# Optimization experiments

Hardware: AMD Instinct MI355X
Metric: run time of the kernel (lower is better)

The kernel has to match this reference:

```python
import jax, jax.numpy as jnp
import numpy as np
from jax import lax

# dims
B, T, C, V, L = 4, 1024, 1024, 32000, 2
NR, NT, E = 6, 2, 8          # rwkv experts, transformer experts, total
HID = 4 * C                  # FFN hidden
P, R = 8, 64                 # bridge prefix_len, low_rank_dim
NH, HD = 16, 64              # heads, head_size


def _layernorm(x, g, b, eps=1e-5):
    m = jnp.mean(x, axis=-1, keepdims=True)
    v = jnp.var(x, axis=-1, keepdims=True)
    return (x - m) * lax.rsqrt(v + eps) * g + b


def setup_inputs() -> dict:
    key = jax.random.key(0)
    ks = list(jax.random.split(key, 32))
    it = iter(ks)
    def nrm(shape, s=0.02):
        return jax.random.normal(next(it), shape, dtype=jnp.float32) * s
    inp = {}
    inp['idx'] = jax.random.randint(next(it), (B, T), 0, V)
    inp['capital_shares'] = jax.random.uniform(next(it), (L, E), dtype=jnp.float32)
    inp['emb'] = nrm((V, C), 1.0)
    inp['head'] = nrm((C, V))
    inp['ln1_g'] = jnp.ones((L, C), jnp.float32)
    inp['ln1_b'] = jnp.zeros((L, C), jnp.float32)
    inp['ln2_g'] = jnp.ones((L, C), jnp.float32)
    inp['ln2_b'] = jnp.zeros((L, C), jnp.float32)
    inp['lno_g'] = jnp.ones((C,), jnp.float32)
    inp['lno_b'] = jnp.zeros((C,), jnp.float32)
    inp['att_Wr'] = nrm((L, C, C))
    inp['att_Wk'] = nrm((L, C, C))
    inp['att_Wv'] = nrm((L, C, C))
    inp['att_Wo'] = nrm((L, C, C))
    inp['att_decay'] = nrm((L, C), 1.0)
    inp['critic_wd'] = nrm((L, C))
    inp['critic_Wa'] = nrm((L, C, E))
    inp['bridge_Wdown'] = nrm((C, R))
    inp['bridge_Wup'] = nrm((P, R, C))
    inp['eWk'] = nrm((L, NR, C, HID))
    inp['eWv'] = nrm((L, NR, HID, C))
    inp['conf_r'] = nrm((L, NR, C))
    inp['tWq'] = nrm((L, NT, C, C))
    inp['tWk'] = nrm((L, NT, C, C))
    inp['tWv'] = nrm((L, NT, C, C))
    inp['tWo'] = nrm((L, NT, C, C))
    inp['conf_t'] = nrm((L, NT, C))
    return inp


def _forward(idx, capital_shares, emb, head, ln1_g, ln1_b, ln2_g, ln2_b,
             lno_g, lno_b, att_Wr, att_Wk, att_Wv, att_Wo, att_decay,
             critic_wd, critic_Wa, bridge_Wdown, bridge_Wup,
             eWk, eWv, conf_r, tWq, tWk, tWv, tWo, conf_t):
    x = emb[idx]                                   # [B,T,C]
    v_first = jnp.zeros_like(x)
    for l in range(L):
        # --- TimeMix (simplified RWKV: per-channel decayed kv state) ---
        x_ln = _layernorm(x, ln1_g[l], ln1_b[l])
        r = jax.nn.sigmoid(x_ln @ att_Wr[l])       # [B,T,C]
        k = x_ln @ att_Wk[l]
        v = x_ln @ att_Wv[l]
        if l == 0:
            v_first = v
        else:
            v = 0.5 * (v + v_first)
        w = jax.nn.sigmoid(att_decay[l])           # [C] decay in (0,1)
        def step(s, kv):
            kt, vt = kv
            s = w * s + kt * vt
            return s, s
        kT = jnp.swapaxes(k, 0, 1)                 # [T,B,C]
        vT = jnp.swapaxes(v, 0, 1)
        _, s_seq = lax.scan(step, jnp.zeros((B, C), x.dtype), (kT, vT))
        rwkv_state = jnp.swapaxes(s_seq, 0, 1)     # [B,T,C]
        att_out = (r * rwkv_state) @ att_Wo[l]
        x = x + att_out
        # --- routing (market) ---
        h = _layernorm(x, ln2_g[l], ln2_b[l])
        conf_rw = jax.nn.sigmoid(jnp.einsum('btc,ec->bte', h, conf_r[l]))
        conf_tr = jax.nn.sigmoid(jnp.einsum('btc,ec->bte', h, conf_t[l]))
        confidences = jnp.concatenate([conf_rw, conf_tr], axis=-1)  # [B,T,E]
        difficulty = jax.nn.softplus(jnp.einsum('btc,c->bt', h, critic_wd[l]))[..., None]
        affinity = jnp.einsum('btc,ce->bte', h, critic_Wa[l])
        subsidy = jnp.tanh(affinity)               # critic.apply_to_bids(0, affinity)
        bids = confidences * capital_shares[l] * difficulty + subsidy
        top2_vals, winners = lax.top_k(bids, 2)    # [B,T,2]
        weights = jax.nn.softmax(top2_vals, axis=-1)
        gate = (weights[..., 0:1] * jax.nn.one_hot(winners[..., 0], E, dtype=h.dtype)
                + weights[..., 1:2] * jax.nn.one_hot(winners[..., 1], E, dtype=h.dtype))  # [B,T,E]
        # --- bridge prefix (low-rank, shared) ---
        flat_h = h.reshape(-1, C)
        flat_state = rwkv_state.reshape(-1, C)
        u = (flat_h + flat_state) @ bridge_Wdown   # [N,R]
        prefix = jnp.einsum('nr,prc->npc', u, bridge_Wup)  # [N,P,C]
        # --- experts: dense-equivalent of gather/compute/scatter ---
        final = jnp.zeros_like(h)
        for e in range(NR):                        # squared-relu FFN experts
            hid = jnp.square(jax.nn.relu(h @ eWk[l, e]))
            final = final + gate[..., e:e + 1] * (hid @ eWv[l, e])
        scale = 1.0 / jnp.sqrt(jnp.float32(HD))
        for j in range(NT):                        # linear transformer experts over prefix
            q = (flat_h @ tWq[l, j]).reshape(-1, NH, HD)
            kp = (prefix @ tWk[l, j]).reshape(-1, P, NH, HD)
            vp = (prefix @ tWv[l, j]).reshape(-1, P, NH, HD)
            attn = jax.nn.softmax(jnp.einsum('nhd,nphd->nhp', q, kp) * scale, axis=-1)
            o = jnp.einsum('nhp,nphd->nhd', attn, vp).reshape(-1, C) @ tWo[l, j]
            final = final + gate[..., NR + j:NR + j + 1] * o.reshape(B, T, C)
        x = x + final
    x = _layernorm(x, lno_g, lno_b)
    return x @ head                                # [B,T,V] logits


def reference(idx, capital_shares, emb, head, ln1_g, ln1_b, ln2_g, ln2_b,
              lno_g, lno_b, att_Wr, att_Wk, att_Wv, att_Wo, att_decay,
              critic_wd, critic_Wa, bridge_Wdown, bridge_Wup,
              eWk, eWv, conf_r, tWq, tWk, tWv, tWo, conf_t):
    return _forward(idx, capital_shares, emb, head, ln1_g, ln1_b, ln2_g, ln2_b,
                    lno_g, lno_b, att_Wr, att_Wk, att_Wv, att_Wo, att_decay,
                    critic_wd, critic_Wa, bridge_Wdown, bridge_Wup,
                    eWk, eWv, conf_r, tWq, tWk, tWv, tWo, conf_t)
```

## Files before the change

kernel.cpp:

```cpp
#include <hip/hip_runtime.h>

typedef _Float16 h16;
typedef __attribute__((ext_vector_type(8))) _Float16 h16x8;
typedef __attribute__((ext_vector_type(4))) _Float16 h16x4;
typedef __attribute__((ext_vector_type(4))) float f32x4;

#define DEVFN static __device__ __forceinline__

DEVFN void gl_lds16(const void* g, void* l) {
  __builtin_amdgcn_global_load_lds((const __attribute__((address_space(1))) unsigned int*)g,
                                   (__attribute__((address_space(3))) unsigned int*)l, 16, 0, 0);
}
DEVFN void fsplit(float v, h16& hi, h16& lo) { hi = (h16)v; lo = (h16)(v - (float)hi); }
DEVFN float wred(float v) {
  #pragma unroll
  for (int m = 32; m >= 1; m >>= 1) v += __shfl_xor(v, m, 64);
  return v;
}
DEVFN float sigm(float x) { return 1.0f / (1.0f + expf(-x)); }
DEVFN float softpl(float x) { return fmaxf(x, 0.0f) + log1pf(expf(-fabsf(x))); }

enum { EPI_WRITE = 0, EPI_ADD = 1, EPI_SQRELU = 3, EPI_TSPLIT = 4, EPI_SCATTER = 5 };

template<bool SPLIT, int EPI, int MODE>
__global__ __launch_bounds__(256, 2) void gemm_k(
    const h16* __restrict__ Ah, const h16* __restrict__ Al, long lda, long sAz,
    const h16* __restrict__ Bh, const h16* __restrict__ Bl, long ldb, long sBz,
    float* __restrict__ C, long ldc, long sCz,
    h16* __restrict__ Oh, h16* __restrict__ Ol, long ldo,
    int K, int nmask, const float* __restrict__ rs, int rsStride,
    const int4* __restrict__ meta, int metaStep,
    const int* __restrict__ lists, int listStep, long sOz)
{
  __shared__ h16 As[(SPLIT ? 2 : 1) * 4096];
  __shared__ h16 Bs[(SPLIT ? 2 : 1) * 4096];
  const int tid = threadIdx.x;
  const int lane = tid & 63, wave = tid >> 6;
  const int wr = wave >> 1, wc = wave & 1;
  const long z = blockIdx.z;
  const long m0 = (long)blockIdx.x * 128, n0 = (long)blockIdx.y * 128;

  int cntv = 0;
  long koff = 0;
  const int* lst = nullptr;
  if (MODE == 1) {
    const int4 mt = meta[z * metaStep];
    if ((int)m0 >= mt.y) return;
    cntv = mt.x; lst = lists + z * listStep;
  } else if (MODE == 2) {
    const int4 mt = meta[0];
    if ((int)m0 >= mt.y) return;
    cntv = mt.x; lst = lists; koff = z * (long)K;
  }

  const h16* pAh = Ah + z * sAz;
  const h16* pBh = Bh + z * sBz;
  const h16* pAl = SPLIT ? (Al + z * sAz) : nullptr;
  const h16* pBl = SPLIT ? (Bl + z * sBz) : nullptr;
  const int rA = wave * 16 + (lane >> 2);
  const int khalf = (lane & 3) * 8;
  long arow0, arow1;
  if (MODE == 1) { arow0 = lst[m0 + rA]; arow1 = lst[m0 + rA + 64]; }
  else           { arow0 = m0 + rA; arow1 = arow0 + 64; }
  const long aoff0 = arow0 * lda + khalf + koff;
  const long aoff1 = arow1 * lda + khalf + koff;
  const long boff = (n0 + rA) * ldb + khalf + koff;
  h16* lA = &As[wave * 512];
  h16* lB = &Bs[wave * 512];
  const int fr = lane & 15, fq = lane >> 4;

  const f32x4 zero = {0.f, 0.f, 0.f, 0.f};
  f32x4 acc[4][4];
  #pragma unroll
  for (int m = 0; m < 4; m++)
    #pragma unroll
    for (int n = 0; n < 4; n++) acc[m][n] = zero;

  for (int k0 = 0; k0 < K; k0 += 32) {
    gl_lds16(pAh + aoff0 + k0, lA);
    gl_lds16(pAh + aoff1 + k0, lA + 2048);
    gl_lds16(pBh + boff + k0, lB);
    gl_lds16(pBh + boff + k0 + 64 * ldb, lB + 2048);
    if (SPLIT) {
      gl_lds16(pAl + aoff0 + k0, lA + 4096);
      gl_lds16(pAl + aoff1 + k0, lA + 4096 + 2048);
      gl_lds16(pBl + boff + k0, lB + 4096);
      gl_lds16(pBl + boff + k0 + 64 * ldb, lB + 4096 + 2048);
    }
    __syncthreads();
    h16x8 af[4], bf[4], afl[4], bfl[4];
    #pragma unroll
    for (int m = 0; m < 4; m++) {
      const int r = (wr * 64 + m * 16 + fr) * 32 + fq * 8;
      af[m] = *(const h16x8*)&As[r];
      if (SPLIT) afl[m] = *(const h16x8*)&As[4096 + r];
    }
    #pragma unroll
    for (int n = 0; n < 4; n++) {
      const int r = (wc * 64 + n * 16 + fr) * 32 + fq * 8;
      bf[n] = *(const h16x8*)&Bs[r];
      if (SPLIT) bfl[n] = *(const h16x8*)&Bs[4096 + r];
    }
    #pragma unroll
    for (int m = 0; m < 4; m++)
      #pragma unroll
      for (int n = 0; n < 4; n++) {
        acc[m][n] = __builtin_amdgcn_mfma_f32_16x16x32_f16(af[m], bf[n], acc[m][n], 0, 0, 0);
        if (SPLIT) {
          acc[m][n] = __builtin_amdgcn_mfma_f32_16x16x32_f16(af[m], bfl[n], acc[m][n], 0, 0, 0);
          acc[m][n] = __builtin_amdgcn_mfma_f32_16x16x32_f16(afl[m], bf[n], acc[m][n], 0, 0, 0);
        }
      }
    __syncthreads();
  }

  #pragma unroll
  for (int m = 0; m < 4; m++) {
    const long lrow = m0 + wr * 64 + m * 16 + fq * 4;
    #pragma unroll
    for (int n = 0; n < 4; n++) {
      const long gcol = n0 + wc * 64 + n * 16 + fr;
      if (nmask && gcol >= nmask) continue;
      if (EPI == EPI_TSPLIT) {
        h16x4 hv, lv;
        #pragma unroll
        for (int i = 0; i < 4; i++) { h16 a, b2; fsplit(acc[m][n][i], a, b2); hv[i] = a; lv[i] = b2; }
        *(h16x4*)&Oh[z * sOz + gcol * ldo + lrow] = hv;
        *(h16x4*)&Ol[z * sOz + gcol * ldo + lrow] = lv;
      } else if (EPI == EPI_SCATTER) {
        #pragma unroll
        for (int i = 0; i < 4; i++) {
          const int slot = (int)lrow + i;
          if (slot >= cntv) continue;
          const int tok = lst[slot];
          const float g = rs[(long)tok * rsStride];
          atomicAdd(&C[(long)tok * ldc + gcol], g * acc[m][n][i]);
        }
      } else {
        float* cp = C + z * sCz + lrow * ldc + gcol;
        #pragma unroll
        for (int i = 0; i < 4; i++) {
          const float v = acc[m][n][i];
          if (EPI == EPI_WRITE) cp[i * ldc] = v;
          else cp[i * ldc] += v;
        }
      }
    }
  }
}

template<bool SPLIT, int EPI, int MODE>
__global__ __launch_bounds__(512, 1) void gemm256_k(
    const h16* __restrict__ Ah, const h16* __restrict__ Al, long lda,
    const h16* __restrict__ Bh, const h16* __restrict__ Bl, long ldb, long sBz,
    float* __restrict__ C, long ldc,
    h16* __restrict__ Oh, h16* __restrict__ Ol, long ldo,
    int K, const float* __restrict__ rs, int rsStride,
    const int4* __restrict__ meta, const int* __restrict__ lists, int listStep,
    const int* __restrict__ mmap)
{
  __shared__ h16 As[(SPLIT ? 2 : 1) * 8192];
  __shared__ h16 Bs[(SPLIT ? 2 : 1) * 8192];
  const int tid = threadIdx.x;
  const int lane = tid & 63, wave = tid >> 6;
  const int wr = wave >> 2, wc = wave & 3;
  const long m0 = (long)blockIdx.x * 256, n0 = (long)blockIdx.y * 256;

  int cntv = 0, eIdx = 0, eOff = 0;
  long koff = 0;
  const int* lst = nullptr;
  if (MODE == 3 || MODE == 4) {
    if ((int)m0 >= meta[8].x) return;
    eIdx = mmap[blockIdx.x];
    const int4 mt = meta[eIdx];
    cntv = mt.x; eOff = mt.z;
    lst = lists + eIdx * listStep;
    if (MODE == 4) koff = blockIdx.z * (long)K;
  }

  const h16* pAh = Ah;
  const h16* pBh = Bh + (long)eIdx * sBz;
  const h16* pAl = SPLIT ? Al : nullptr;
  const h16* pBl = SPLIT ? (Bl + (long)eIdx * sBz) : nullptr;
  const int rA = (tid >> 2) & 127;
  const int khalf = (lane & 3) * 8;
  long arow0, arow1;
  if (MODE == 3) { arow0 = lst[m0 + rA - eOff]; arow1 = lst[m0 + rA + 128 - eOff]; }
  else           { arow0 = m0 + rA; arow1 = arow0 + 128; }
  const long aoff0 = arow0 * lda + khalf + koff;
  const long aoff1 = arow1 * lda + khalf + koff;
  const long boff0 = (n0 + rA) * ldb + khalf + koff;
  const long boff1 = boff0 + 128 * ldb;
  h16* lA = &As[wave * 512];
  h16* lB = &Bs[wave * 512];
  const int fr = lane & 15, fq = lane >> 4;

  const f32x4 zero = {0.f, 0.f, 0.f, 0.f};
  f32x4 acc[8][4];
  #pragma unroll
  for (int m = 0; m < 8; m++)
    #pragma unroll
    for (int n = 0; n < 4; n++) acc[m][n] = zero;

  for (int k0 = 0; k0 < K; k0 += 32) {
    gl_lds16(pAh + aoff0 + k0, lA);
    gl_lds16(pAh + aoff1 + k0, lA + 4096);
    gl_lds16(pBh + boff0 + k0, lB);
    gl_lds16(pBh + boff1 + k0, lB + 4096);
    if (SPLIT) {
      gl_lds16(pAl + aoff0 + k0, lA + 8192);
      gl_lds16(pAl + aoff1 + k0, lA + 8192 + 4096);
      gl_lds16(pBl + boff0 + k0, lB + 8192);
      gl_lds16(pBl + boff1 + k0, lB + 8192 + 4096);
    }
    __syncthreads();
    h16x8 bf[4], bfl[4];
    #pragma unroll
    for (int n = 0; n < 4; n++) {
      const int r = (wc * 64 + n * 16 + fr) * 32 + fq * 8;
      bf[n] = *(const h16x8*)&Bs[r];
      if (SPLIT) bfl[n] = *(const h16x8*)&Bs[8192 + r];
    }
    #pragma unroll
    for (int m = 0; m < 8; m++) {
      const int r = (wr * 128 + m * 16 + fr) * 32 + fq * 8;
      const h16x8 af = *(const h16x8*)&As[r];
      h16x8 afl;
      if (SPLIT) afl = *(const h16x8*)&As[8192 + r];
      #pragma unroll
      for (int n = 0; n < 4; n++) {
        acc[m][n] = __builtin_amdgcn_mfma_f32_16x16x32_f16(af, bf[n], acc[m][n], 0, 0, 0);
        if (SPLIT) {
          acc[m][n] = __builtin_amdgcn_mfma_f32_16x16x32_f16(af, bfl[n], acc[m][n], 0, 0, 0);
          acc[m][n] = __builtin_amdgcn_mfma_f32_16x16x32_f16(afl, bf[n], acc[m][n], 0, 0, 0);
        }
      }
    }
    __syncthreads();
  }

  #pragma unroll
  for (int m = 0; m < 8; m++) {
    const long lrow = m0 + wr * 128 + m * 16 + fq * 4;
    #pragma unroll
    for (int n = 0; n < 4; n++) {
      const long gcol = n0 + wc * 64 + n * 16 + fr;
      if (EPI == EPI_SQRELU) {
        #pragma unroll
        for (int i = 0; i < 4; i++) {
          float v = acc[m][n][i];
          v = v > 0.f ? v * v : 0.f;
          const h16 a = (h16)v;
          Oh[(lrow + i) * ldo + gcol] = a;
          if (Ol) Ol[(lrow + i) * ldo + gcol] = (h16)(v - (float)a);
        }
      } else if (EPI == EPI_SCATTER) {
        #pragma unroll
        for (int i = 0; i < 4; i++) {
          const int slot = (int)lrow + i - eOff;
          if (slot >= cntv) continue;
          const int tok = lst[slot];
          atomicAdd(&C[(long)tok * ldc + gcol], rs[(long)tok * rsStride + eIdx] * acc[m][n][i]);
        }
      } else {
        float* cp = C + lrow * ldc + gcol;
        #pragma unroll
        for (int i = 0; i < 4; i++) cp[i * ldc] = acc[m][n][i];
      }
    }
  }
}

template<bool LO>
__global__ __launch_bounds__(256) void k_tsplit(
    const float* __restrict__ in, long inZ,
    h16* __restrict__ oh, h16* __restrict__ ol, long outZ, int Kd, int Nd)
{
  __shared__ float t[64][65];
  const long z = blockIdx.z;
  in += z * inZ; oh += z * outZ; if (LO) ol += z * outZ;
  const int n0 = blockIdx.x * 64, k0 = blockIdx.y * 64;
  const int tr = threadIdx.x >> 4, tc = threadIdx.x & 15;
  #pragma unroll
  for (int r = 0; r < 4; r++) {
    const int row = r * 16 + tr;
    const float4 v = *(const float4*)&in[(long)(k0 + row) * Nd + n0 + tc * 4];
    t[row][tc * 4 + 0] = v.x; t[row][tc * 4 + 1] = v.y;
    t[row][tc * 4 + 2] = v.z; t[row][tc * 4 + 3] = v.w;
  }
  __syncthreads();
  #pragma unroll
  for (int r = 0; r < 4; r++) {
    const int nrow = r * 16 + tr;
    h16x4 hv, lv;
    #pragma unroll
    for (int i = 0; i < 4; i++) {
      h16 a, b2; fsplit(t[tc * 4 + i][nrow], a, b2);
      hv[i] = a; lv[i] = b2;
    }
    *(h16x4*)&oh[(long)(n0 + nrow) * Kd + k0 + tc * 4] = hv;
    if (LO) *(h16x4*)&ol[(long)(n0 + nrow) * Kd + k0 + tc * 4] = lv;
  }
}

template<bool LO>
__global__ __launch_bounds__(256) void k_tsplit4(
    const float* __restrict__ s0, const float* __restrict__ s1,
    const float* __restrict__ s2, const float* __restrict__ s3,
    long inAdd, h16* __restrict__ oh, h16* __restrict__ ol, int Kd, int Nd)
{
  __shared__ float t[64][65];
  const int z = blockIdx.z;
  const long seg = (long)Kd * Nd;
  const int w = z & 3;
  const float* in = (w == 0 ? s0 : w == 1 ? s1 : w == 2 ? s2 : s3) + (inAdd + (z >> 2)) * seg;
  oh += (long)z * seg; if (LO) ol += (long)z * seg;
  const int n0 = blockIdx.x * 64, k0 = blockIdx.y * 64;
  const int tr = threadIdx.x >> 4, tc = threadIdx.x & 15;
  #pragma unroll
  for (int r = 0; r < 4; r++) {
    const int row = r * 16 + tr;
    const float4 v = *(const float4*)&in[(long)(k0 + row) * Nd + n0 + tc * 4];
    t[row][tc * 4 + 0] = v.x; t[row][tc * 4 + 1] = v.y;
    t[row][tc * 4 + 2] = v.z; t[row][tc * 4 + 3] = v.w;
  }
  __syncthreads();
  #pragma unroll
  for (int r = 0; r < 4; r++) {
    const int nrow = r * 16 + tr;
    h16x4 hv, lv;
    #pragma unroll
    for (int i = 0; i < 4; i++) {
      h16 a, b2; fsplit(t[tc * 4 + i][nrow], a, b2);
      hv[i] = a; lv[i] = b2;
    }
    *(h16x4*)&oh[(long)(n0 + nrow) * Kd + k0 + tc * 4] = hv;
    if (LO) *(h16x4*)&ol[(long)(n0 + nrow) * Kd + k0 + tc * 4] = lv;
  }
}

__global__ void k_split(const float* __restrict__ in, h16* __restrict__ oh, h16* __restrict__ ol)
{
  const long i = (long)blockIdx.x * 256 + threadIdx.x;
  const float4 v = ((const float4*)in)[i];
  h16x4 hv, lv; h16 a, b2;
  fsplit(v.x, a, b2); hv[0] = a; lv[0] = b2;
  fsplit(v.y, a, b2); hv[1] = a; lv[1] = b2;
  fsplit(v.z, a, b2); hv[2] = a; lv[2] = b2;
  fsplit(v.w, a, b2); hv[3] = a; lv[3] = b2;
  ((h16x4*)oh)[i] = hv; ((h16x4*)ol)[i] = lv;
}

__global__ void k_embed(const int* __restrict__ idx, const float* __restrict__ emb, float* __restrict__ x)
{
  const int row = blockIdx.x;
  const long e = (long)idx[row] * 1024;
  ((float4*)(x + (long)row * 1024))[threadIdx.x] = ((const float4*)(emb + e))[threadIdx.x];
}

__global__ __launch_bounds__(256) void k_ln(
    const float* __restrict__ x, const float* __restrict__ g, const float* __restrict__ b,
    float* __restrict__ yf, h16* __restrict__ yh, h16* __restrict__ yl)
{
  const int row = blockIdx.x, tid = threadIdx.x;
  const float4 v = ((const float4*)(x + (long)row * 1024))[tid];
  __shared__ float red[4];
  const int wv = tid >> 6;
  float s = wred(v.x + v.y + v.z + v.w);
  if ((tid & 63) == 0) red[wv] = s;
  __syncthreads();
  const float mean = (red[0] + red[1] + red[2] + red[3]) * (1.0f / 1024.0f);
  const float d0 = v.x - mean, d1 = v.y - mean, d2 = v.z - mean, d3 = v.w - mean;
  float s2 = wred(d0 * d0 + d1 * d1 + d2 * d2 + d3 * d3);
  __syncthreads();
  if ((tid & 63) == 0) red[wv] = s2;
  __syncthreads();
  const float var = (red[0] + red[1] + red[2] + red[3]) * (1.0f / 1024.0f);
  const float rstd = 1.0f / sqrtf(var + 1e-5f);
  const float4 gv = ((const float4*)g)[tid];
  const float4 bv = ((const float4*)b)[tid];
  const float y0 = d0 * rstd * gv.x + bv.x;
  const float y1 = d1 * rstd * gv.y + bv.y;
  const float y2 = d2 * rstd * gv.z + bv.z;
  const float y3 = d3 * rstd * gv.w + bv.w;
  if (yf) { float4 o; o.x = y0; o.y = y1; o.z = y2; o.w = y3; ((float4*)(yf + (long)row * 1024))[tid] = o; }
  h16x4 hv, lv; h16 a, b2;
  fsplit(y0, a, b2); hv[0] = a; lv[0] = b2;
  fsplit(y1, a, b2); hv[1] = a; lv[1] = b2;
  fsplit(y2, a, b2); hv[2] = a; lv[2] = b2;
  fsplit(y3, a, b2); hv[3] = a; lv[3] = b2;
  *(h16x4*)(yh + (long)row * 1024 + tid * 4) = hv;
  if (yl) *(h16x4*)(yl + (long)row * 1024 + tid * 4) = lv;
}

__global__ void k_vfix(float* __restrict__ rkv, float* __restrict__ vfir, int mode)
{
  const int row = blockIdx.x, tid = threadIdx.x;
  float4* vp = (float4*)(rkv + (long)row * 3072 + 2048) + tid;
  float4* fp = (float4*)(vfir + (long)row * 1024) + tid;
  if (mode == 0) *fp = *vp;
  else {
    float4 a = *vp; const float4 b = *fp;
    a.x = 0.5f * (a.x + b.x); a.y = 0.5f * (a.y + b.y);
    a.z = 0.5f * (a.z + b.z); a.w = 0.5f * (a.w + b.w);
    *vp = a;
  }
}

__global__ __launch_bounds__(256) void k_scan1(const float* __restrict__ rkv,
                                               const float* __restrict__ dec, float* __restrict__ carry)
{
  const int gid = blockIdx.x * 256 + threadIdx.x;
  const int c = gid & 1023, bb = (gid >> 10) & 3, ch = gid >> 12;
  const float w = sigm(dec[c]);
  float s = 0.f;
  const long base = ((long)bb * 1024 + ch * 64) * 3072 + c;
  const float* kp_ = rkv + 1024 + base;
  const float* vp_ = rkv + 2048 + base;
  for (int t = 0; t < 64; t++) s = w * s + kp_[(long)t * 3072] * vp_[(long)t * 3072];
  carry[(ch * 4 + bb) * 1024 + c] = s;
}
__global__ void k_scan2(const float* __restrict__ dec, float* __restrict__ carry)
{
  const int gid = blockIdx.x * 256 + threadIdx.x;
  const int c = gid & 1023, bb = gid >> 10;
  const float w = sigm(dec[c]);
  float w64 = w;
  for (int i = 0; i < 6; i++) w64 *= w64;
  float s = 0.f;
  for (int j = 0; j < 16; j++) {
    const int o = (j * 4 + bb) * 1024 + c;
    const float a = carry[o];
    carry[o] = s;
    s = w64 * s + a;
  }
}
__global__ __launch_bounds__(256) void k_scan3(const float* __restrict__ rkv,
                                               const float* __restrict__ dec, const float* __restrict__ carry,
                                               float* __restrict__ st)
{
  const int gid = blockIdx.x * 256 + threadIdx.x;
  const int c = gid & 1023, bb = (gid >> 10) & 3, ch = gid >> 12;
  const float w = sigm(dec[c]);
  float s = carry[(ch * 4 + bb) * 1024 + c];
  const long base = ((long)bb * 1024 + ch * 64) * 3072 + c;
  const float* kp_ = rkv + 1024 + base;
  const float* vp_ = rkv + 2048 + base;
  float* so = st + ((long)bb * 1024 + ch * 64) * 1024 + c;
  for (int t = 0; t < 64; t++) {
    s = w * s + kp_[(long)t * 3072] * vp_[(long)t * 3072];
    so[(long)t * 1024] = s;
  }
}

__global__ void k_attin(const float* __restrict__ rkv, const float* __restrict__ s,
                        h16* __restrict__ oh, h16* __restrict__ ol)
{
  const int row = blockIdx.x, tid = threadIdx.x;
  const float4 rv = *((const float4*)(rkv + (long)row * 3072) + tid);
  const float4 sv = *((const float4*)(s + (long)row * 1024) + tid);
  h16x4 hv, lv; h16 a, b2;
  fsplit(sv.x * sigm(rv.x), a, b2); hv[0] = a; lv[0] = b2;
  fsplit(sv.y * sigm(rv.y), a, b2); hv[1] = a; lv[1] = b2;
  fsplit(sv.z * sigm(rv.z), a, b2); hv[2] = a; lv[2] = b2;
  fsplit(sv.w * sigm(rv.w), a, b2); hv[3] = a; lv[3] = b2;
  const long i = (long)row * 256 + tid;
  ((h16x4*)oh)[i] = hv; ((h16x4*)ol)[i] = lv;
}

__global__ void k_addsplit(const float* __restrict__ p, const float* __restrict__ q,
                           h16* __restrict__ oh, h16* __restrict__ ol)
{
  const long i = (long)blockIdx.x * 256 + threadIdx.x;
  const float4 av = ((const float4*)p)[i];
  const float4 bv = ((const float4*)q)[i];
  h16x4 hv, lv; h16 a, b2;
  fsplit(av.x + bv.x, a, b2); hv[0] = a; lv[0] = b2;
  fsplit(av.y + bv.y, a, b2); hv[1] = a; lv[1] = b2;
  fsplit(av.z + bv.z, a, b2); hv[2] = a; lv[2] = b2;
  fsplit(av.w + bv.w, a, b2); hv[3] = a; lv[3] = b2;
  ((h16x4*)oh)[i] = hv; ((h16x4*)ol)[i] = lv;
}

__global__ __launch_bounds__(256) void k_route(
    const float* __restrict__ h, const float* __restrict__ cr, const float* __restrict__ ct,
    const float* __restrict__ wd, const float* __restrict__ wa,
    const float* __restrict__ cap, float* __restrict__ gate)
{
  const int wv = threadIdx.x >> 6, ln = threadIdx.x & 63;
  const int row = blockIdx.x * 4 + wv;
  const float* hr = h + (long)row * 1024;
  float hreg[16];
  #pragma unroll
  for (int i = 0; i < 4; i++) {
    const float4 t = ((const float4*)hr)[ln * 4 + i];
    hreg[i * 4 + 0] = t.x; hreg[i * 4 + 1] = t.y; hreg[i * 4 + 2] = t.z; hreg[i * 4 + 3] = t.w;
  }
  float dots[17];
  #pragma unroll
  for (int e = 0; e < 6; e++) {
    float p = 0.f;
    #pragma unroll
    for (int j = 0; j < 16; j++) p += hreg[j] * cr[e * 1024 + ln * 16 + j];
    dots[e] = p;
  }
  #pragma unroll
  for (int e = 0; e < 2; e++) {
    float p = 0.f;
    #pragma unroll
    for (int j = 0; j < 16; j++) p += hreg[j] * ct[e * 1024 + ln * 16 + j];
    dots[6 + e] = p;
  }
  {
    float p = 0.f;
    #pragma unroll
    for (int j = 0; j < 16; j++) p += hreg[j] * wd[ln * 16 + j];
    dots[8] = p;
  }
  #pragma unroll
  for (int e = 0; e < 8; e++) {
    float p = 0.f;
    #pragma unroll
    for (int j = 0; j < 16; j++) p += hreg[j] * wa[(ln * 16 + j) * 8 + e];
    dots[9 + e] = p;
  }
  #pragma unroll
  for (int d = 0; d < 17; d++) dots[d] = wred(dots[d]);
  if (ln == 0) {
    float bids[8];
    const float diff = softpl(dots[8]);
    #pragma unroll
    for (int e = 0; e < 6; e++) bids[e] = sigm(dots[e]) * cap[e] * diff + tanhf(dots[9 + e]);
    #pragma unroll
    for (int e = 0; e < 2; e++) bids[6 + e] = sigm(dots[6 + e]) * cap[6 + e] * diff + tanhf(dots[15 + e]);
    int w0 = 0;
    for (int e = 1; e < 8; e++) if (bids[e] > bids[w0]) w0 = e;
    int w1 = -1;
    for (int e = 0; e < 8; e++) if (e != w0 && (w1 < 0 || bids[e] > bids[w1])) w1 = e;
    const float e1 = expf(bids[w1] - bids[w0]);
    const float q0 = 1.0f / (1.0f + e1), q1 = e1 / (1.0f + e1);
    for (int e = 0; e < 8; e++) gate[(long)row * 8 + e] = (e == w0) ? q0 : ((e == w1) ? q1 : 0.0f);
  }
}

__global__ void k_build(const float* __restrict__ gate, int* __restrict__ cnt, int* __restrict__ lists)
{
  const int t = blockIdx.x * 256 + threadIdx.x;
  #pragma unroll
  for (int e = 0; e < 8; e++)
    if (gate[(long)t * 8 + e] > 0.f) { const int s = atomicAdd(&cnt[e], 1); lists[e * 4224 + s] = t; }
}
__global__ void k_meta(const int* __restrict__ cnt, int4* __restrict__ meta, int* __restrict__ lists,
                       int* __restrict__ mmap)
{
  __shared__ int sc[8], sp[8], so[8];
  if (threadIdx.x == 0) {
    int acc = 0;
    for (int e = 0; e < 8; e++) {
      const int c = cnt[e], p = (c + 255) & ~255;
      sc[e] = c; sp[e] = p; so[e] = (e < 6) ? acc : 0;
      if (e < 6) acc += p;
    }
    meta[8] = make_int4(acc, 0, 0, 0);
    for (int b = 0; b < 64; b++) mmap[b] = 0;
    for (int e = 0; e < 6; e++)
      for (int b = so[e] >> 8; b < (so[e] + sp[e]) >> 8; b++) mmap[b] = e;
  }
  __syncthreads();
  const int e = threadIdx.x >> 5, i = threadIdx.x & 31;
  for (int s = sc[e] + i; s < sp[e]; s += 32) lists[e * 4224 + s] = 0;
  if (i == 0) meta[e] = make_int4(sc[e], sp[e], so[e], 0);
}

__global__ __launch_bounds__(256) void k_scores(const float* __restrict__ q, const float* __restrict__ kp,
                                                float* __restrict__ attn, const int4* __restrict__ meta)
{
  const int gw = blockIdx.x * 4 + (threadIdx.x >> 6), ln = threadIdx.x & 63;
  const int n = gw >> 4, hh = gw & 15;
  if (n >= meta->y) return;
  const float qv = q[(long)n * 1024 + hh * 64 + ln];
  float s[8];
  #pragma unroll
  for (int p = 0; p < 8; p++) {
    float t = qv * kp[(long)n * 8192 + p * 1024 + hh * 64 + ln];
    s[p] = wred(t) * 0.125f;
  }
  if (ln == 0) {
    float mx = s[0];
    #pragma unroll
    for (int p = 1; p < 8; p++) mx = fmaxf(mx, s[p]);
    float ex[8], sum = 0.f;
    #pragma unroll
    for (int p = 0; p < 8; p++) { ex[p] = expf(s[p] - mx); sum += ex[p]; }
    const float inv = 1.0f / sum;
    #pragma unroll
    for (int p = 0; p < 8; p++) attn[(long)n * 128 + hh * 8 + p] = ex[p] * inv;
  }
}

__global__ void k_omix(const float* __restrict__ attn, const float* __restrict__ vp,
                       h16* __restrict__ oh, h16* __restrict__ ol, const int4* __restrict__ meta)
{
  const long gid = (long)blockIdx.x * 256 + threadIdx.x;
  const int n = gid >> 10, hd = gid & 1023, hh = hd >> 6;
  if (n >= meta->y) return;
  const float* a = attn + (long)n * 128 + hh * 8;
  float o = 0.f;
  #pragma unroll
  for (int p = 0; p < 8; p++) o += a[p] * vp[(long)n * 8192 + p * 1024 + hd];
  h16 hi, lo; fsplit(o, hi, lo);
  oh[gid] = hi; ol[gid] = lo;
}

#define GEMM3(SPL, EPI, MODE, GRID, ...) do { \
  if (SPL) gemm_k<true,  EPI, MODE><<<GRID, 256, 0, stream>>>(__VA_ARGS__); \
  else     gemm_k<false, EPI, MODE><<<GRID, 256, 0, stream>>>(__VA_ARGS__); } while (0)
#define GEMM256(SPL, EPI, MODE, GRID, ...) do { \
  if (SPL) gemm256_k<true,  EPI, MODE><<<GRID, 512, 0, stream>>>(__VA_ARGS__); \
  else     gemm256_k<false, EPI, MODE><<<GRID, 512, 0, stream>>>(__VA_ARGS__); } while (0)

extern "C" void kernel_launch(void* const* d_in, const int* in_sizes, int n_in,
                              void* d_out, int out_size, void* d_ws, size_t ws_size,
                              hipStream_t stream)
{
  (void)in_sizes; (void)n_in; (void)out_size; (void)ws_size;
  const int*   idx   = (const int*)  d_in[0];
  const float* cap   = (const float*)d_in[1];
  const float* emb   = (const float*)d_in[2];
  const float* headw = (const float*)d_in[3];
  const float* ln1g  = (const float*)d_in[4];
  const float* ln1b  = (const float*)d_in[5];
  const float* ln2g  = (const float*)d_in[6];
  const float* ln2b  = (const float*)d_in[7];
  const float* lnog  = (const float*)d_in[8];
  const float* lnob  = (const float*)d_in[9];
  const float* aWr   = (const float*)d_in[10];
  const float* aWk   = (const float*)d_in[11];
  const float* aWv   = (const float*)d_in[12];
  const float* aWo   = (const float*)d_in[13];
  const float* adec  = (const float*)d_in[14];
  const float* cwd   = (const float*)d_in[15];
  const float* cWa   = (const float*)d_in[16];
  const float* bWd   = (const float*)d_in[17];
  const float* bWu   = (const float*)d_in[18];
  const float* eWkw  = (const float*)d_in[19];
  const float* eWvw  = (const float*)d_in[20];
  const float* confr = (const float*)d_in[21];
  const float* tWq   = (const float*)d_in[22];
  const float* tWkk  = (const float*)d_in[23];
  const float* tWv   = (const float*)d_in[24];
  const float* tWo   = (const float*)d_in[25];
  const float* conft = (const float*)d_in[26];
  float* out = (float*)d_out;

  char* ws = (char*)d_ws;
  size_t off = 0;
  auto alloc = [&](size_t n) -> char* {
    off = (off + 255) & ~(size_t)255;
    char* p = ws + off; off += n; return p;
  };
  const long M1 = 1048576, M4 = 4194304;

  h16* attWh = (h16*)alloc(8 * M1 * 2);
  h16* attWl = (h16*)alloc(8 * M1 * 2);
  h16* eWkh  = (h16*)alloc(12 * M4 * 2);
  h16* eWkl  = (h16*)alloc(6 * M4 * 2);
  h16* eWvh  = (h16*)alloc(12 * M4 * 2);
  h16* eWvl  = (h16*)alloc(6 * M4 * 2);
  h16* tWh   = (h16*)alloc(16 * M1 * 2);
  h16* headh = (h16*)alloc(32768000ull * 2);
  h16* wdh   = (h16*)alloc(131072 * 2);
  h16* wuph  = (h16*)alloc(524288 * 2);
  h16* wupl  = (h16*)alloc(524288 * 2);
  h16* wukth = (h16*)alloc(524288 * 2);
  h16* wuvth = (h16*)alloc(524288 * 2);
  h16* wuktl = (h16*)alloc(524288 * 2);
  h16* wuvtl = (h16*)alloc(524288 * 2);
  h16* s1h   = (h16*)alloc(M4 * 2);
  h16* s1l   = (h16*)alloc(M4 * 2);
  h16* hh_   = (h16*)alloc(M4 * 2);
  h16* hl_   = (h16*)alloc(M4 * 2);
  h16* uh    = (h16*)alloc(262144 * 2);
  h16* ul    = (h16*)alloc(262144 * 2);
  float* x    = (float*)alloc(M4 * 4);
  float* vfir = (float*)alloc(M4 * 4);
  float* rkv  = (float*)alloc(3 * M4 * 4);
  float* st   = (float*)alloc(M4 * 4);
  float* hf   = (float*)alloc(M4 * 4);
  float* qf   = (float*)alloc(M4 * 4);
  char* big   = alloc(167772160);
  h16* hidh   = (h16*)big;
  h16* hidl   = (h16*)(big + 83886080ull);
  float* kp   = (float*)big;
  float* carry = (float*)alloc(65536 * 4);
  float* gate  = (float*)alloc(32768 * 4);
  float* uf    = (float*)alloc(262144 * 4);
  float* attn  = (float*)alloc(524288 * 4);
  int*   cnt8  = (int*)alloc(32);
  int4*  metaA = (int4*)alloc(16 * 16);
  int*   lists = (int*)alloc(8 * 4224 * 4);
  int*   mmap  = (int*)alloc(64 * 4);

  k_tsplit4<true><<<dim3(16, 16, 8), 256, 0, stream>>>(aWr, aWk, aWv, aWo, 0, attWh, attWl, 1024, 1024);
  k_tsplit<true ><<<dim3(64, 16, 6), 256, 0, stream>>>(eWkw, M4, eWkh, eWkl, M4, 1024, 4096);
  k_tsplit<false><<<dim3(64, 16, 6), 256, 0, stream>>>(eWkw + 6 * M4, M4, eWkh + 6 * M4, nullptr, M4, 1024, 4096);
  k_tsplit<true ><<<dim3(16, 64, 6), 256, 0, stream>>>(eWvw, M4, eWvh, eWvl, M4, 4096, 1024);
  k_tsplit<false><<<dim3(16, 64, 6), 256, 0, stream>>>(eWvw + 6 * M4, M4, eWvh + 6 * M4, nullptr, M4, 4096, 1024);
  k_tsplit4<false><<<dim3(16, 16, 16), 256, 0, stream>>>(tWq, tWkk, tWv, tWo, 0, tWh, nullptr, 1024, 1024);
  k_tsplit<false><<<dim3(500, 16, 1), 256, 0, stream>>>(headw, 0, headh, nullptr, 0, 1024, 32000);
  k_tsplit<false><<<dim3(1, 16, 1), 256, 0, stream>>>(bWd, 0, wdh, nullptr, 0, 1024, 64);
  hipMemsetAsync(wdh + 65536, 0, 65536 * 2, stream);
  k_split<<<512, 256, 0, stream>>>(bWu, wuph, wupl);

  k_embed<<<4096, 256, 0, stream>>>(idx, emb, x);

  for (int l = 0; l < 2; l++) {
    const bool SE = (l == 0);
    k_ln<<<4096, 256, 0, stream>>>(x, ln1g + l * 1024, ln1b + l * 1024, nullptr, s1h, s1l);
    GEMM3(true, EPI_WRITE, 0, dim3(32, 24),
          s1h, s1l, 1024, 0, attWh + (l * 4) * M1, attWl + (l * 4) * M1, 1024, 0,
          rkv, 3072, 0, nullptr, nullptr, 0, 1024, 0, nullptr, 0, nullptr, 0, nullptr, 0, 0);
    k_vfix<<<4096, 256, 0, stream>>>(rkv, vfir, l == 0 ? 0 : 1);
    k_scan1<<<256, 256, 0, stream>>>(rkv, adec + l * 1024, carry);
    k_scan2<<<16, 256, 0, stream>>>(adec + l * 1024, carry);
    k_scan3<<<256, 256, 0, stream>>>(rkv, adec + l * 1024, carry, st);
    k_attin<<<4096, 256, 0, stream>>>(rkv, st, s1h, s1l);
    GEMM3(true, EPI_ADD, 0, dim3(32, 8),
          s1h, s1l, 1024, 0, attWh + (l * 4 + 3) * M1, attWl + (l * 4 + 3) * M1, 1024, 0,
          x, 1024, 0, nullptr, nullptr, 0, 1024, 0, nullptr, 0, nullptr, 0, nullptr, 0, 0);
    k_ln<<<4096, 256, 0, stream>>>(x, ln2g + l * 1024, ln2b + l * 1024, hf, hh_, hl_);
    k_route<<<1024, 256, 0, stream>>>(hf, confr + l * 6144, conft + l * 2048, cwd + l * 1024, cWa + l * 8192, cap + l * 8, gate);
    hipMemsetAsync(cnt8, 0, 32, stream);
    k_build<<<16, 256, 0, stream>>>(gate, cnt8, lists);
    k_meta<<<1, 256, 0, stream>>>(cnt8, metaA, lists, mmap);
    k_addsplit<<<4096, 256, 0, stream>>>(hf, st, s1h, s1l);
    GEMM3(false, EPI_WRITE, 0, dim3(32, 1),
          s1h, nullptr, 1024, 0, wdh, nullptr, 1024, 0,
          uf, 64, 0, nullptr, nullptr, 0, 1024, 64, nullptr, 0, nullptr, 0, nullptr, 0, 0);
    k_split<<<256, 256, 0, stream>>>(uf, uh, ul);
    GEMM256(SE, EPI_SQRELU, 3, dim3(40, 16),
            hh_, hl_, 1024, eWkh + l * 6 * M4, eWkl, 1024, M4,
            nullptr, 0, hidh, SE ? hidl : nullptr, 4096,
            1024, nullptr, 0, metaA, lists, 4224, mmap);
    GEMM256(SE, EPI_SCATTER, 4, dim3(40, 4, 4),
            hidh, hidl, 4096, eWvh + l * 6 * M4, eWvl, 4096, M4,
            x, 1024, nullptr, nullptr, 0,
            1024, gate, 8, metaA, lists, 4224, mmap);
    for (int j = 0; j < 2; j++) {
      const long wi = (l * 2 + j) * 4;
      const int4* mt = metaA + 6 + j;
      const int* lstT = lists + (6 + j) * 4224;
      GEMM3(false, EPI_TSPLIT, 0, dim3(4, 8, 2),
            wuph, nullptr, 1024, 0, tWh + (wi + 1) * M1, nullptr, 1024, M1,
            nullptr, 0, 0, wukth, wuktl, 512, 1024, 0, nullptr, 0, nullptr, 0, nullptr, 0, 524288);
      GEMM3(false, EPI_WRITE, 1, dim3(32, 8),
            hh_, nullptr, 1024, 0, tWh + (wi + 0) * M1, nullptr, 1024, 0,
            qf, 1024, 0, nullptr, nullptr, 0, 1024, 0, nullptr, 0, mt, 0, lstT, 0, 0);
      GEMM3(false, EPI_WRITE, 1, dim3(32, 8, 8),
            uh, nullptr, 64, 0, wukth, nullptr, 512, 64,
            kp, 8192, 1024, nullptr, nullptr, 0, 64, 0, nullptr, 0, mt, 0, lstT, 0, 0);
      k_scores<<<16384, 256, 0, stream>>>(qf, kp, attn, mt);
      GEMM3(false, EPI_WRITE, 1, dim3(32, 8, 8),
            uh, nullptr, 64, 0, wuvth, nullptr, 512, 64,
            kp, 8192, 1024, nullptr, nullptr, 0, 64, 0, nullptr, 0, mt, 0, lstT, 0, 0);
      k_omix<<<16384, 256, 0, stream>>>(attn, kp, s1h, s1l, mt);
      GEMM3(false, EPI_SCATTER, 2, dim3(32, 8, 4),
            s1h, nullptr, 1024, 0, tWh + (wi + 3) * M1, nullptr, 1024, 0,
            x, 1024, 0, nullptr, nullptr, 0, 256, 0, gate + 6 + j, 8, mt, 0, lstT, 0, 0);
    }
  }

  k_ln<<<4096, 256, 0, stream>>>(x, lnog, lnob, nullptr, s1h, s1l);
  GEMM3(false, EPI_WRITE, 0, dim3(32, 250),
        s1h, nullptr, 1024, 0, headh, nullptr, 1024, 0,
        out, 32000, 0, nullptr, nullptr, 0, 1024, 0, nullptr, 0, nullptr, 0, nullptr, 0, 0);
}
```

Measured before the change: 2.954 ms.

## Batch both transformer experts into single launches with fp16 intermediates

Replaces the per-expert loop for the two transformer experts with batched GEMM launches that cover both experts through new grid-z modes, which cut the number of kernel launches and raise the number of blocks per launch. The prefix K/V projections are now written as fp16 instead of fp32, and the attention output is stored as fp16 only, with no hi/lo split. The RWKV down-projection split-K count is also doubled. The fp16 storage of K, V and the attention output lowers precision, and the change adds more atomic scatter traffic.

New measurement: 3.184 ms. 1.08x slower.

```diff
diff --git a/kernel.cpp b/kernel.cpp
--- a/kernel.cpp
+++ b/kernel.cpp
@@ -20,7 +20,7 @@
 DEVFN float sigm(float x) { return 1.0f / (1.0f + expf(-x)); }
 DEVFN float softpl(float x) { return fmaxf(x, 0.0f) + log1pf(expf(-fabsf(x))); }
 
-enum { EPI_WRITE = 0, EPI_ADD = 1, EPI_SQRELU = 3, EPI_TSPLIT = 4, EPI_SCATTER = 5 };
+enum { EPI_WRITE = 0, EPI_ADD = 1, EPI_SQRELU = 3, EPI_TSPLIT = 4, EPI_SCATTER = 5, EPI_WRITEH = 6 };
 
 template<bool SPLIT, int EPI, int MODE>
 __global__ __launch_bounds__(256, 2) void gemm_k(
@@ -40,7 +40,7 @@
   const long z = blockIdx.z;
   const long m0 = (long)blockIdx.x * 128, n0 = (long)blockIdx.y * 128;
 
-  int cntv = 0;
+  int cntv = 0, eSel = 0;
   long koff = 0;
   const int* lst = nullptr;
   if (MODE == 1) {
@@ -51,20 +51,36 @@
     const int4 mt = meta[0];
     if ((int)m0 >= mt.y) return;
     cntv = mt.x; lst = lists; koff = z * (long)K;
-  }
-
-  const h16* pAh = Ah + z * sAz;
-  const h16* pBh = Bh + z * sBz;
-  const h16* pAl = SPLIT ? (Al + z * sAz) : nullptr;
-  const h16* pBl = SPLIT ? (Bl + z * sBz) : nullptr;
+  } else if (MODE == 5) {
+    eSel = (int)(z >> 2);
+    const int4 mt = meta[eSel * metaStep];
+    if ((int)m0 >= mt.y) return;
+    cntv = mt.x; lst = lists + eSel * listStep;
+    koff = (long)(z & 3) * K;
+  } else if (MODE == 6) {
+    eSel = (int)(z >> 3);
+    const int4 mt = meta[eSel * metaStep];
+    if ((int)m0 >= mt.y) return;
+    cntv = mt.x; lst = lists + eSel * listStep;
+  }
+
+  long zA = z, zB = z;
+  if (MODE == 5) { zA = eSel; zB = eSel; }
+  else if (MODE == 6) { zA = eSel; }
+  const h16* pAh = Ah + zA * sAz;
+  const h16* pBh = Bh + zB * sBz;
+  const h16* pAl = SPLIT ? (Al + zA * sAz) : nullptr;
+  const h16* pBl = SPLIT ? (Bl + zB * sBz) : nullptr;
   const int rA = wave * 16 + (lane >> 2);
   const int khalf = (lane & 3) * 8;
   long arow0, arow1;
-  if (MODE == 1) { arow0 = lst[m0 + rA]; arow1 = lst[m0 + rA + 64]; }
-  else           { arow0 = m0 + rA; arow1 = arow0 + 64; }
-  const long aoff0 = arow0 * lda + khalf + koff;
-  const long aoff1 = arow1 * lda + khalf + koff;
+  if (MODE == 1 || MODE == 6) { arow0 = lst[m0 + rA]; arow1 = lst[m0 + rA + 64]; }
+  else if (MODE == 5)         { arow0 = m0 + rA; arow1 = arow0 + 64; }
+  else                        { arow0 = m0 + rA; arow1 = arow0 + 64; }
+  const long aoff0 = arow0 * lda + khalf + (MODE == 5 ? 0 : koff);
+  const long aoff1 = arow1 * lda + khalf + (MODE == 5 ? 0 : koff);
   const long boff = (n0 + rA) * ldb + khalf + koff;
+  const long aoffk = (MODE == 5 ? koff : 0);
   h16* lA = &As[wave * 512];
   h16* lB = &Bs[wave * 512];
   const int fr = lane & 15, fq = lane >> 4;
@@ -77,13 +93,13 @@
     for (int n = 0; n < 4; n++) acc[m][n] = zero;
 
   for (int k0 = 0; k0 < K; k0 += 32) {
-    gl_lds16(pAh + aoff0 + k0, lA);
-    gl_lds16(pAh + aoff1 + k0, lA + 2048);
+    gl_lds16(pAh + aoff0 + aoffk + k0, lA);
+    gl_lds16(pAh + aoff1 + aoffk + k0, lA + 2048);
     gl_lds16(pBh + boff + k0, lB);
     gl_lds16(pBh + boff + k0 + 64 * ldb, lB + 2048);
     if (SPLIT) {
-      gl_lds16(pAl + aoff0 + k0, lA + 4096);
-      gl_lds16(pAl + aoff1 + k0, lA + 4096 + 2048);
+      gl_lds16(pAl + aoff0 + aoffk + k0, lA + 4096);
+      gl_lds16(pAl + aoff1 + aoffk + k0, lA + 4096 + 2048);
       gl_lds16(pBl + boff + k0, lB + 4096);
       gl_lds16(pBl + boff + k0 + 64 * ldb, lB + 4096 + 2048);
     }
@@ -127,13 +143,17 @@
         for (int i = 0; i < 4; i++) { h16 a, b2; fsplit(acc[m][n][i], a, b2); hv[i] = a; lv[i] = b2; }
         *(h16x4*)&Oh[z * sOz + gcol * ldo + lrow] = hv;
         *(h16x4*)&Ol[z * sOz + gcol * ldo + lrow] = lv;
+      } else if (EPI == EPI_WRITEH) {
+        #pragma unroll
+        for (int i = 0; i < 4; i++)
+          Oh[z * sOz + (lrow + i) * ldo + gcol] = (h16)acc[m][n][i];
       } else if (EPI == EPI_SCATTER) {
         #pragma unroll
         for (int i = 0; i < 4; i++) {
           const int slot = (int)lrow + i;
           if (slot >= cntv) continue;
           const int tok = lst[slot];
-          const float g = rs[(long)tok * rsStride];
+          const float g = rs[(long)tok * rsStride + (MODE == 5 ? eSel : 0)];
           atomicAdd(&C[(long)tok * ldc + gcol], g * acc[m][n][i]);
         }
       } else {
@@ -572,7 +592,7 @@
   if (i == 0) meta[e] = make_int4(sc[e], sp[e], so[e], 0);
 }
 
-__global__ __launch_bounds__(256) void k_scores(const float* __restrict__ q, const float* __restrict__ kp,
+__global__ __launch_bounds__(256) void k_scores(const float* __restrict__ q, const h16* __restrict__ kp,
                                                 float* __restrict__ attn, const int4* __restrict__ meta)
 {
   const int gw = blockIdx.x * 4 + (threadIdx.x >> 6), ln = threadIdx.x & 63;
@@ -582,7 +602,7 @@
   float s[8];
   #pragma unroll
   for (int p = 0; p < 8; p++) {
-    float t = qv * kp[(long)n * 8192 + p * 1024 + hh * 64 + ln];
+    float t = qv * (float)kp[(long)p * 4194304 + (long)n * 1024 + hh * 64 + ln];
     s[p] = wred(t) * 0.125f;
   }
   if (ln == 0) {
@@ -598,8 +618,8 @@
   }
 }
 
-__global__ void k_omix(const float* __restrict__ attn, const float* __restrict__ vp,
-                       h16* __restrict__ oh, h16* __restrict__ ol, const int4* __restrict__ meta)
+__global__ void k_omix2(const float* __restrict__ attn, const h16* __restrict__ vp,
+                        h16* __restrict__ oh, const int4* __restrict__ meta)
 {
   const long gid = (long)blockIdx.x * 256 + threadIdx.x;
   const int n = gid >> 10, hd = gid & 1023, hh = hd >> 6;
@@ -607,9 +627,8 @@
   const float* a = attn + (long)n * 128 + hh * 8;
   float o = 0.f;
   #pragma unroll
-  for (int p = 0; p < 8; p++) o += a[p] * vp[(long)n * 8192 + p * 1024 + hd];
-  h16 hi, lo; fsplit(o, hi, lo);
-  oh[gid] = hi; ol[gid] = lo;
+  for (int p = 0; p < 8; p++) o += a[p] * (float)vp[(long)p * 4194304 + (long)n * 1024 + hd];
+  oh[gid] = (h16)o;
 }
 
 #define GEMM3(SPL, EPI, MODE, GRID, ...) do { \
@@ -672,11 +691,11 @@
   h16* wdh   = (h16*)alloc(131072 * 2);
   h16* wuph  = (h16*)alloc(524288 * 2);
   h16* wupl  = (h16*)alloc(524288 * 2);
-  h16* wukth = (h16*)alloc(524288 * 2);
-  h16* wuvth = (h16*)alloc(524288 * 2);
-  h16* wuktl = (h16*)alloc(524288 * 2);
-  h16* wuvtl = (h16*)alloc(524288 * 2);
-  h16* s1h   = (h16*)alloc(M4 * 2);
+  h16* foldKh = (h16*)alloc(1048576 * 2);
+  h16* foldKl = (h16*)alloc(1048576 * 2);
+  h16* foldVh = (h16*)alloc(1048576 * 2);
+  h16* foldVl = (h16*)alloc(1048576 * 2);
+  h16* s1h   = (h16*)alloc(2 * M4 * 2);
   h16* s1l   = (h16*)alloc(M4 * 2);
   h16* hh_   = (h16*)alloc(M4 * 2);
   h16* hl_   = (h16*)alloc(M4 * 2);
@@ -687,15 +706,15 @@
   float* rkv  = (float*)alloc(3 * M4 * 4);
   float* st   = (float*)alloc(M4 * 4);
   float* hf   = (float*)alloc(M4 * 4);
-  float* qf   = (float*)alloc(M4 * 4);
+  float* qf   = (float*)alloc(2 * M4 * 4);
   char* big   = alloc(167772160);
   h16* hidh   = (h16*)big;
   h16* hidl   = (h16*)(big + 83886080ull);
-  float* kp   = (float*)big;
+  h16* kpH    = (h16*)big;
   float* carry = (float*)alloc(65536 * 4);
   float* gate  = (float*)alloc(32768 * 4);
   float* uf    = (float*)alloc(262144 * 4);
-  float* attn  = (float*)alloc(524288 * 4);
+  float* attn  = (float*)alloc(2 * 524288 * 4);
   int*   cnt8  = (int*)alloc(32);
   int4*  metaA = (int4*)alloc(16 * 16);
   int*   lists = (int*)alloc(8 * 4224 * 4);
@@ -742,32 +761,38 @@
             hh_, hl_, 1024, eWkh + l * 6 * M4, eWkl, 1024, M4,
             nullptr, 0, hidh, SE ? hidl : nullptr, 4096,
             1024, nullptr, 0, metaA, lists, 4224, mmap);
-    GEMM256(SE, EPI_SCATTER, 4, dim3(40, 4, 4),
+    GEMM256(SE, EPI_SCATTER, 4, dim3(40, 4, 8),
             hidh, hidl, 4096, eWvh + l * 6 * M4, eWvl, 4096, M4,
             x, 1024, nullptr, nullptr, 0,
-            1024, gate, 8, metaA, lists, 4224, mmap);
-    for (int j = 0; j < 2; j++) {
-      const long wi = (l * 2 + j) * 4;
-      const int4* mt = metaA + 6 + j;
-      const int* lstT = lists + (6 + j) * 4224;
-      GEMM3(false, EPI_TSPLIT, 0, dim3(4, 8, 2),
-            wuph, nullptr, 1024, 0, tWh + (wi + 1) * M1, nullptr, 1024, M1,
-            nullptr, 0, 0, wukth, wuktl, 512, 1024, 0, nullptr, 0, nullptr, 0, nullptr, 0, 524288);
-      GEMM3(false, EPI_WRITE, 1, dim3(32, 8),
-            hh_, nullptr, 1024, 0, tWh + (wi + 0) * M1, nullptr, 1024, 0,
-            qf, 1024, 0, nullptr, nullptr, 0, 1024, 0, nullptr, 0, mt, 0, lstT, 0, 0);
-      GEMM3(false, EPI_WRITE, 1, dim3(32, 8, 8),
-            uh, nullptr, 64, 0, wukth, nullptr, 512, 64,
-            kp, 8192, 1024, nullptr, nullptr, 0, 64, 0, nullptr, 0, mt, 0, lstT, 0, 0);
-      k_scores<<<16384, 256, 0, stream>>>(qf, kp, attn, mt);
-      GEMM3(false, EPI_WRITE, 1, dim3(32, 8, 8),
-            uh, nullptr, 64, 0, wuvth, nullptr, 512, 64,
-            kp, 8192, 1024, nullptr, nullptr, 0, 64, 0, nullptr, 0, mt, 0, lstT, 0, 0);
-      k_omix<<<16384, 256, 0, stream>>>(attn, kp, s1h, s1l, mt);
-      GEMM3(false, EPI_SCATTER, 2, dim3(32, 8, 4),
-            s1h, nullptr, 1024, 0, tWh + (wi + 3) * M1, nullptr, 1024, 0,
-            x, 1024, 0, nullptr, nullptr, 0, 256, 0, gate + 6 + j, 8, mt, 0, lstT, 0, 0);
-    }
+            512, gate, 8, metaA, lists, 4224, mmap);
+    GEMM3(false, EPI_TSPLIT, 0, dim3(4, 8, 2),
+          wuph, nullptr, 1024, 0, tWh + (l * 8 + 1) * M1, nullptr, 1024, 4 * M1,
+          nullptr, 0, 0, foldKh, foldKl, 1024, 1024, 0, nullptr, 0, nullptr, 0, nullptr, 0, 512);
+    GEMM3(false, EPI_TSPLIT, 0, dim3(4, 8, 2),
+          wuph, nullptr, 1024, 0, tWh + (l * 8 + 2) * M1, nullptr, 1024, 4 * M1,
+          nullptr, 0, 0, foldVh, foldVl, 1024, 1024, 0, nullptr, 0, nullptr, 0, nullptr, 0, 512);
+    GEMM3(false, EPI_WRITE, 1, dim3(32, 8, 2),
+          hh_, nullptr, 1024, 0, tWh + (l * 8 + 0) * M1, nullptr, 1024, 4 * M1,
+          qf, 1024, M4, nullptr, nullptr, 0, 1024, 0, nullptr, 0,
+          metaA + 6, 1, lists + 6 * 4224, 4224, 0);
+    GEMM3(false, EPI_WRITEH, 6, dim3(32, 8, 16),
+          uh, nullptr, 64, 0, foldKh, nullptr, 1024, 64,
+          nullptr, 0, 0, kpH, nullptr, 1024, 64, 0, nullptr, 0,
+          metaA + 6, 1, lists + 6 * 4224, 4224, M4);
+    for (int j = 0; j < 2; j++)
+      k_scores<<<16384, 256, 0, stream>>>(qf + (long)j * M4, kpH + (long)j * 8 * M4,
+                                          attn + (long)j * 524288, metaA + 6 + j);
+    GEMM3(false, EPI_WRITEH, 6, dim3(32, 8, 16),
+          uh, nullptr, 64, 0, foldVh, nullptr, 1024, 64,
+          nullptr, 0, 0, kpH, nullptr, 1024, 64, 0, nullptr, 0,
+          metaA + 6, 1, lists + 6 * 4224, 4224, M4);
+    for (int j = 0; j < 2; j++)
+      k_omix2<<<16384, 256, 0, stream>>>(attn + (long)j * 524288, kpH + (long)j * 8 * M4,
+                                         s1h + (long)j * M4, metaA + 6 + j);
+    GEMM3(false, EPI_SCATTER, 5, dim3(32, 8, 8),
+          s1h, nullptr, 1024, M4, tWh + (l * 8 + 3) * M1, nullptr, 1024, 4 * M1,
+          x, 1024, 0, nullptr, nullptr, 0, 256, 0, gate + 6, 8,
+          metaA + 6, 1, lists + 6 * 4224, 4224, 0);
   }
 
   k_ln<<<4096, 256, 0, stream>>>(x, lnog, lnob, nullptr, s1h, s1l);
```
